# Kernel optimization log

Hardware: AMD Instinct MI355X
Metric: run time of the kernel (lower is better)

The kernel has to match this reference:

```python
import jax, jax.numpy as jnp
import numpy as np

NUM_HEADS = 12
NUM_GROUPS = 4
METRIC_SCALE = 1.0
CLS_MIX = 1.0
MEAN_MIX = 0.5
ROUTER_SCALE = 1.0
DIFF_SCALE = 1.0
B, N, D, HF = 16, 577, 768, 3072


def _ln(x, g, b, eps=1e-5):
    mu = jnp.mean(x, axis=-1, keepdims=True)
    var = jnp.mean(jnp.square(x - mu), axis=-1, keepdims=True)
    return (x - mu) * jax.lax.rsqrt(var + eps) * g + b


def setup_inputs() -> dict:
    key = jax.random.key(0)
    ks = iter(jax.random.split(key, 16))
    w = lambda shape, std: jax.random.normal(next(ks), shape, jnp.float32) * std
    return {
        "x": w((B, N, D), 1.0),
        "ln1_g": jnp.ones((D,)), "ln1_b": jnp.zeros((D,)),
        "ad_ln_g": jnp.ones((D,)), "ad_ln_b": jnp.zeros((D,)),
        "ad_w": w((D, D), 0.02),
        "w_qkv": w((D, 3 * D), 0.02),
        "w_proj": w((D, D), 0.02), "b_proj": jnp.zeros((D,)),
        "ln2_g": jnp.ones((D,)), "ln2_b": jnp.zeros((D,)),
        "fc1_w": w((D, HF), 0.02), "fc1_b": jnp.zeros((HF,)),
        "fc2_w": w((HF, D), 0.02), "fc2_b": jnp.zeros((D,)),
        "r_ln_g": jnp.ones((HF,)), "r_ln_b": jnp.zeros((HF,)),
        "r_proj_w": w((2 * HF, NUM_GROUPS), 0.02), "r_proj_b": jnp.zeros((NUM_GROUPS,)),
        "r_gate_w": w((2 * HF, 1), 0.02), "r_gate_b": jnp.full((1,), -2.0),
        "r_scale": jnp.full((NUM_GROUPS,), 0.1),
        "d_ln_g": jnp.ones((HF,)), "d_ln_b": jnp.zeros((HF,)),
        "d_out_w": w((HF, HF), 0.005),
        "d_gate_w": w((HF, 1), 0.02), "d_gate_b": jnp.full((1,), -1.5),
    }


def reference(x, ln1_g, ln1_b, ad_ln_g, ad_ln_b, ad_w, w_qkv, w_proj, b_proj,
              ln2_g, ln2_b, fc1_w, fc1_b, fc2_w, fc2_b,
              r_ln_g, r_ln_b, r_proj_w, r_proj_b, r_gate_w, r_gate_b, r_scale,
              d_ln_g, d_ln_b, d_out_w, d_gate_w, d_gate_b):
    b, n, d = x.shape
    hd = d // NUM_HEADS
    # ---- GeoAttention (pre-norm) ----
    h = _ln(x, ln1_g, ln1_b)
    # metric adapter: residual LN+Linear (SharedAttentionMetricAdapter)
    metric_h = h + METRIC_SCALE * (_ln(h, ad_ln_g, ad_ln_b) @ ad_w)
    # q,k from metric path; v from plain path (asymmetric Q/K vs V)
    qk = metric_h @ w_qkv[:, : 2 * d]                # [b,n,2d]
    v = h @ w_qkv[:, 2 * d :]                        # [b,n,d]
    q = qk[..., :d].reshape(b, n, NUM_HEADS, hd).transpose(0, 2, 1, 3)
    k = qk[..., d:].reshape(b, n, NUM_HEADS, hd).transpose(0, 2, 1, 3)
    v = v.reshape(b, n, NUM_HEADS, hd).transpose(0, 2, 1, 3)
    attn = jax.nn.softmax(jnp.einsum("bhnd,bhmd->bhnm", q, k) * (hd ** -0.5), axis=-1)
    out = jnp.einsum("bhnm,bhmd->bhnd", attn, v).transpose(0, 2, 1, 3).reshape(b, n, d)
    x = x + out @ w_proj + b_proj
    # ---- GeoMlp (pre-norm) ----
    h2 = _ln(x, ln2_g, ln2_b)
    hid = h2 @ fc1_w + fc1_b                         # [b,n,HF]
    # GroupCompetitionRouter on hidden
    rn = _ln(hid, r_ln_g, r_ln_b)
    summary = jnp.concatenate([CLS_MIX * rn[:, 0], MEAN_MIX * jnp.mean(rn[:, 1:], axis=1)], axis=-1)  # [b,2HF]
    wts = jax.nn.softmax(summary @ r_proj_w + r_proj_b, axis=-1)       # [b,G]
    gate = jax.nn.sigmoid(summary @ r_gate_w + r_gate_b)               # [b,1]
    centered = wts * float(NUM_GROUPS) - 1.0
    grouped = hid.reshape(b, n, NUM_GROUPS, HF // NUM_GROUPS)
    scale = 1.0 + ROUTER_SCALE * gate[:, None, :, None] * r_scale[None, None, :, None] * centered[:, None, :, None]
    hid = (grouped * scale).reshape(b, n, HF)
    # TokenDiffusionMixer on hidden
    dn = _ln(hid, d_ln_g, d_ln_b)
    tr = dn / jnp.maximum(jnp.linalg.norm(dn, axis=-1, keepdims=True), 1e-12)
    aff = jax.nn.softmax(jnp.einsum("bnc,bmc->bnm", tr, tr) * (HF ** -0.5), axis=-1)
    diffusion = jnp.einsum("bnm,bmc->bnc", aff, dn) - dn
    dgate = jax.nn.sigmoid(dn[:, 0] @ d_gate_w + d_gate_b)             # [b,1]
    hid = hid + DIFF_SCALE * dgate[:, :, None] * (diffusion @ d_out_w)
    # activation + fc2
    hid = jax.nn.gelu(hid, approximate=False)
    return x + hid @ fc2_w + fc2_b
```

## Files before the change

kernel.cpp:

```cpp
#include <hip/hip_runtime.h>
#include <math.h>

typedef unsigned short u16;
typedef unsigned int   u32;
typedef __attribute__((ext_vector_type(4))) float f32x4;
typedef __attribute__((ext_vector_type(4))) u32   u32x4;
typedef __attribute__((ext_vector_type(8))) short s16x8;

#define DEV __device__ __forceinline__
#define AS1 __attribute__((address_space(1)))
#define AS3 __attribute__((address_space(3)))

DEV float b2f(u16 u){ u32 x = ((u32)u)<<16; float f; __builtin_memcpy(&f,&x,4); return f; }
DEV u16 f2b(float f){ u32 x; __builtin_memcpy(&x,&f,4); u32 r = x + 0x7FFFu + ((x>>16)&1u); return (u16)(r>>16); }

DEV float ldf(const float* p, long i){ return p[i]; }
DEV float ldf(const u16*   p, long i){ return b2f(p[i]); }

DEV void gload16(const u16* g, u16* l){
  __builtin_amdgcn_global_load_lds((const AS1 u32*)(const void*)g,
                                   (AS3 u32*)(void*)l, 16, 0, 0);
}

DEV float wave_sum(float v){
#pragma unroll
  for(int o=32;o;o>>=1) v += __shfl_down(v,o,64);
  return v;
}
DEV float wave_max(float v){
#pragma unroll
  for(int o=32;o;o>>=1) v = fmaxf(v, __shfl_down(v,o,64));
  return v;
}
DEV float block_sum(float v, float* tmp){
  v = wave_sum(v);
  if((threadIdx.x&63)==0) tmp[threadIdx.x>>6]=v;
  __syncthreads();
  float r = tmp[0]+tmp[1]+tmp[2]+tmp[3];
  __syncthreads();
  return r;
}
DEV float block_max(float v, float* tmp){
  v = wave_max(v);
  if((threadIdx.x&63)==0) tmp[threadIdx.x>>6]=v;
  __syncthreads();
  float r = fmaxf(fmaxf(tmp[0],tmp[1]),fmaxf(tmp[2],tmp[3]));
  __syncthreads();
  return r;
}

template<typename TI>
__global__ void transpose_pad(const TI* __restrict__ in, u16* __restrict__ out,
                              int R, int C, int Rpad, long strideI, long strideO){
  __shared__ u16 t[32][33];
  in  += (long)blockIdx.z*strideI;
  out += (long)blockIdx.z*strideO;
  int tx = threadIdx.x & 31, ty = threadIdx.x >> 5;
  int bc = blockIdx.x*32, br = blockIdx.y*32;
#pragma unroll
  for(int i=0;i<32;i+=8){
    int r = br+ty+i, c = bc+tx;
    float v = (r<R && c<C) ? ldf(in,(long)r*C+c) : 0.f;
    t[ty+i][tx] = f2b(v);
  }
  __syncthreads();
#pragma unroll
  for(int i=0;i<32;i+=8){
    int c = bc+ty+i, r = br+tx;
    if(c<C && r<Rpad) out[(long)c*Rpad + r] = t[tx][ty+i];
  }
}

template<typename TI>
__global__ void ln_rows(const TI* __restrict__ x, const float* __restrict__ g,
                        const float* __restrict__ b, u16* __restrict__ y, int W){
  __shared__ float tmp[4];
  long base=(long)blockIdx.x*W;
  float s=0.f, ss=0.f;
  for(int c=threadIdx.x;c<W;c+=256){ float v=ldf(x,base+c); s+=v; ss+=v*v; }
  s=block_sum(s,tmp); ss=block_sum(ss,tmp);
  float mu=s/W;
  float rstd=rsqrtf(fmaxf(ss/W-mu*mu,0.f)+1e-5f);
  for(int c=threadIdx.x;c<W;c+=256){
    float v=ldf(x,base+c);
    y[base+c]=f2b((v-mu)*rstd*g[c]+b[c]);
  }
}

__global__ void ln2_rows(const float* __restrict__ x,
                         const float* __restrict__ g1, const float* __restrict__ b1,
                         const float* __restrict__ g2, const float* __restrict__ b2,
                         u16* __restrict__ h, u16* __restrict__ lnh){
  __shared__ float tmp[4];
  __shared__ float row[768];
  long base=(long)blockIdx.x*768;
  float s=0.f, ss=0.f;
  for(int c=threadIdx.x;c<768;c+=256){ float v=x[base+c]; s+=v; ss+=v*v; }
  s=block_sum(s,tmp); ss=block_sum(ss,tmp);
  float mu=s*(1.f/768.f);
  float rstd=rsqrtf(fmaxf(ss*(1.f/768.f)-mu*mu,0.f)+1e-5f);
  float s2=0.f, ss2=0.f;
  for(int c=threadIdx.x;c<768;c+=256){
    float v=(x[base+c]-mu)*rstd*g1[c]+b1[c];
    row[c]=v; h[base+c]=f2b(v);
    s2+=v; ss2+=v*v;
  }
  s2=block_sum(s2,tmp); ss2=block_sum(ss2,tmp);
  float mu2=s2*(1.f/768.f);
  float rstd2=rsqrtf(fmaxf(ss2*(1.f/768.f)-mu2*mu2,0.f)+1e-5f);
  for(int c=threadIdx.x;c<768;c+=256){
    lnh[base+c]=f2b((row[c]-mu2)*rstd2*g2[c]+b2[c]);
  }
}

__global__ void row_stats(const u16* __restrict__ x, float* __restrict__ stats, int W){
  __shared__ float tmp[4];
  long base=(long)blockIdx.x*W;
  float s=0.f,ss=0.f;
  for(int c=threadIdx.x;c<W;c+=256){ float v=b2f(x[base+c]); s+=v; ss+=v*v; }
  s=block_sum(s,tmp); ss=block_sum(ss,tmp);
  if(threadIdx.x==0){
    float mu=s/W;
    stats[2*(long)blockIdx.x]=mu;
    stats[2*(long)blockIdx.x+1]=rsqrtf(fmaxf(ss/W-mu*mu,0.f)+1e-5f);
  }
}

__global__ void dn_kernel(const u16* __restrict__ x, const float* __restrict__ g,
                          const float* __restrict__ b, const float* __restrict__ scalef,
                          u16* __restrict__ dn, float* __restrict__ rn){
  const int W=3072;
  __shared__ float tmp[4];
  __shared__ u16 rowb[3072];
  long row=(long)blockIdx.x;
  long base=row*(long)W;
  int bz=(int)(row/577);
  float s=0.f,ss=0.f;
  for(int c=threadIdx.x;c<W;c+=256){
    float sc=scalef[bz*4 + ((c>>8)/3)];
    float v=b2f(x[base+c])*sc;
    rowb[c]=f2b(v);
    s+=v; ss+=v*v;
  }
  s=block_sum(s,tmp); ss=block_sum(ss,tmp);
  float mu=s/W;
  float rstd=rsqrtf(fmaxf(ss/W-mu*mu,0.f)+1e-5f);
  float sq=0.f;
  for(int c=threadIdx.x;c<W;c+=256){
    float v=(b2f(rowb[c])-mu)*rstd*g[c]+b[c];
    sq+=v*v;
  }
  sq=block_sum(sq,tmp);
  float r=1.f/fmaxf(sqrtf(sq),1e-12f);
  for(int c=threadIdx.x;c<W;c+=256){
    float v=(b2f(rowb[c])-mu)*rstd*g[c]+b[c];
    dn[base+c]=f2b(v);
  }
  if(threadIdx.x==0) rn[blockIdx.x]=r;
}

__global__ void softmax_rows(u16* __restrict__ S, int W, int Wp,
                             const float* __restrict__ rs, int rpb, float alpha){
  __shared__ float tmp[4];
  long row = blockIdx.x;
  u16* p = S + row*(long)Wp;
  float rowscale = alpha;
  const float* rsb = nullptr;
  if(rs){ long bt=row/rpb; int m=(int)(row%rpb); rsb = rs + bt*(long)rpb; rowscale *= rsb[m]; }
  float mx=-3e38f;
  for(int c=threadIdx.x;c<W;c+=256){
    float v=b2f(p[c])*rowscale; if(rs) v*=rsb[c];
    mx=fmaxf(mx,v);
  }
  mx=block_max(mx,tmp);
  float sm=0.f;
  for(int c=threadIdx.x;c<W;c+=256){
    float v=b2f(p[c])*rowscale; if(rs) v*=rsb[c];
    sm+=__expf(v-mx);
  }
  sm=block_sum(sm,tmp);
  float inv=1.f/sm;
  for(int c=threadIdx.x;c<W;c+=256){
    float v=b2f(p[c])*rowscale; if(rs) v*=rsb[c];
    p[c]=f2b(__expf(v-mx)*inv);
  }
  for(int c=W+threadIdx.x;c<Wp;c+=256) p[c]=0;
}

__global__ void split_heads(const u16* __restrict__ qk, u16* __restrict__ qh, u16* __restrict__ kh){
  int i = blockIdx.x*256+threadIdx.x;
  if(i >= 16*577*12*8) return;
  int dv = i&7; int h=(i>>3)%12; int bn=i/96;
  int b=bn/577, n=bn%577;
  long src=(long)bn*1536 + h*64 + dv*8;
  long dst=((long)((b*12+h)*577+n))*64 + dv*8;
  *(u32x4*)(qh+dst) = *(const u32x4*)(qk+src);
  *(u32x4*)(kh+dst) = *(const u32x4*)(qk+src+768);
}
__global__ void merge_heads(const u16* __restrict__ aoh, u16* __restrict__ aout){
  int i = blockIdx.x*256+threadIdx.x;
  if(i >= 16*577*12*8) return;
  int dv=i&7; int h=(i>>3)%12; int bn=i/96;
  int b=bn/577, n=bn%577;
  long dst=(long)bn*768 + h*64 + dv*8;
  long src=((long)((b*12+h)*577+n))*64 + dv*8;
  *(u32x4*)(aout+dst) = *(const u32x4*)(aoh+src);
}
__global__ void make_vT(const u16* __restrict__ v, u16* __restrict__ vT){
  long i = (long)blockIdx.x*256+threadIdx.x;
  if(i >= (long)192*64*608) return;
  int n=(int)(i%608); long q=i/608; int d=(int)(q&63); int bh=(int)(q>>6);
  int b=bh/12, h=bh%12;
  u16 val=0;
  if(n<577) val = v[((long)(b*577+n))*768 + h*64 + d];
  vT[i]=val;
}

__global__ void summary_kernel(const u16* __restrict__ hid, const float* __restrict__ stats,
                               const float* __restrict__ rg, const float* __restrict__ rb,
                               float* __restrict__ summ){
  int b=blockIdx.y;
  int c=blockIdx.x*256+threadIdx.x;
  const u16* hb=hid+(size_t)b*577*3072;
  const float* st=stats+(size_t)b*577*2;
  float g=rg[c], be=rb[c];
  float cls=(b2f(hb[c])-st[0])*st[1]*g+be;
  float acc=0.f;
#pragma unroll 4
  for(int n=1;n<577;n++) acc += (b2f(hb[(size_t)n*3072+c])-st[2*n])*st[2*n+1];
  summ[(size_t)b*6144+c]        = 1.0f*cls;
  summ[(size_t)b*6144+3072+c]   = 0.5f*(g*(acc*(1.f/576.f))+be);
}

__global__ void router_kernel(const float* __restrict__ summ, const float* __restrict__ pw,
                              const float* __restrict__ pb, const float* __restrict__ gw,
                              const float* __restrict__ gb, const float* __restrict__ rsc,
                              float* __restrict__ scalef){
  __shared__ float tmp[4];
  int b=blockIdx.x;
  float a0=0,a1=0,a2=0,a3=0,a4=0;
  for(int c=threadIdx.x;c<6144;c+=256){
    float sv=summ[(size_t)b*6144+c];
    a0+=sv*pw[c*4+0]; a1+=sv*pw[c*4+1]; a2+=sv*pw[c*4+2]; a3+=sv*pw[c*4+3];
    a4+=sv*gw[c];
  }
  a0=block_sum(a0,tmp); a1=block_sum(a1,tmp); a2=block_sum(a2,tmp);
  a3=block_sum(a3,tmp); a4=block_sum(a4,tmp);
  if(threadIdx.x==0){
    float l0=a0+pb[0], l1=a1+pb[1], l2=a2+pb[2], l3=a3+pb[3];
    float mx=fmaxf(fmaxf(l0,l1),fmaxf(l2,l3));
    float e0=__expf(l0-mx),e1=__expf(l1-mx),e2=__expf(l2-mx),e3=__expf(l3-mx);
    float s=e0+e1+e2+e3;
    float gate=1.f/(1.f+__expf(-(a4+gb[0])));
    float w0=e0/s,w1=e1/s,w2=e2/s,w3=e3/s;
    scalef[b*4+0]=1.f+gate*rsc[0]*(4.f*w0-1.f);
    scalef[b*4+1]=1.f+gate*rsc[1]*(4.f*w1-1.f);
    scalef[b*4+2]=1.f+gate*rsc[2]*(4.f*w2-1.f);
    scalef[b*4+3]=1.f+gate*rsc[3]*(4.f*w3-1.f);
  }
}

__global__ void dgate_kernel(const u16* __restrict__ dn, const float* __restrict__ gw,
                             const float* __restrict__ gb, float* __restrict__ dgate){
  __shared__ float tmp[4];
  int b=blockIdx.x;
  const u16* row = dn + (size_t)b*577*3072;
  float a=0.f;
  for(int c=threadIdx.x;c<3072;c+=256) a+=b2f(row[c])*gw[c];
  a=block_sum(a,tmp);
  if(threadIdx.x==0) dgate[b]=1.f/(1.f+__expf(-(a+gb[0])));
}

constexpr int F_BIAS=1, F_RES=2, F_GELU=4, F_GATE=8, F_RESF32=16, F_OUTF32=32, F_SCRES=64;

DEV int swz(int u){ int row=u>>2, sl=u&3; return row*4 + (sl ^ ((row>>1)&3)); }

template<int FLAGS>
__global__ __launch_bounds__(256,2) void gemm_bt(
  const u16* __restrict__ A, long lda, long szA,
  const u16* __restrict__ B, long ldb, long szB,
  void* __restrict__ Cv, long ldc, long szC,
  const float* __restrict__ bias,
  const void* __restrict__ resv, long ldr, long szR, float res_scale,
  const float* __restrict__ gate,
  float alpha, int M, int N, int K, int NX, int NY)
{
  __shared__ alignas(16) u16 shA[128*32];
  __shared__ alignas(16) u16 shB[128*32];
  const int nwg = (int)gridDim.x;
  const int orig = (int)blockIdx.x;
  const int q = nwg>>3, r = nwg&7;
  const int xcd = orig&7, idx = orig>>3;
  const int wg = (xcd<r ? xcd*(q+1) : r*(q+1)+(xcd-r)*q) + idx;
  const int by = wg % NY; const int t_ = wg / NY;
  const int bx = t_ % NX; const int z  = t_ / NX;

  A += (long)z*szA; B += (long)z*szB;
  const int tid=threadIdx.x, lane=tid&63, wid=tid>>6;
  const int wr=wid>>1, wc=wid&1;
  const long m0=(long)bx*128, n0=(long)by*128;
  f32x4 acc[4][4];
#pragma unroll
  for(int i=0;i<4;i++)
#pragma unroll
    for(int j=0;j<4;j++){ f32x4 zv={0.f,0.f,0.f,0.f}; acc[i][j]=zv; }

  const int lr = lane>>2, lsl = lane&3;
  const u16* pA[2]; const u16* pB[2]; u16* lA[2]; u16* lB[2];
#pragma unroll
  for(int i=0;i<2;i++){
    int ra = wid*32 + i*16 + lr;
    int kc = (lsl ^ ((ra>>1)&3))*8;
    long gr = m0+ra; if(gr>=M) gr=M-1;
    long gb = n0+ra; if(gb>=N) gb=N-1;
    pA[i] = A + gr*lda + kc;
    pB[i] = B + gb*ldb + kc;
    lA[i] = shA + (wid*32 + i*16)*32;
    lB[i] = shB + (wid*32 + i*16)*32;
  }

  for(int k0=0;k0<K;k0+=32){
    __syncthreads();
#pragma unroll
    for(int i=0;i<2;i++){
      gload16(pA[i]+k0, lA[i]);
      gload16(pB[i]+k0, lB[i]);
    }
    __syncthreads();
    const int ks = lane>>4, rr = lane&15;
    s16x8 av[4], bv[4];
#pragma unroll
    for(int mi=0;mi<4;mi++) av[mi] = ((const s16x8*)shA)[swz((wr*64+mi*16+rr)*4+ks)];
#pragma unroll
    for(int ni=0;ni<4;ni++) bv[ni] = ((const s16x8*)shB)[swz((wc*64+ni*16+rr)*4+ks)];
#pragma unroll
    for(int mi=0;mi<4;mi++)
#pragma unroll
      for(int ni=0;ni<4;ni++)
        acc[mi][ni] = __builtin_amdgcn_mfma_f32_16x16x32_bf16(av[mi], bv[ni], acc[mi][ni], 0,0,0);
  }
  const float* resf = (const float*)resv + (long)z*szR;
  const u16*   resh = (const u16*)resv   + (long)z*szR;
  float* Cf = (float*)Cv + (long)z*szC;
  u16*   Ch = (u16*)Cv   + (long)z*szC;
  float gv = (FLAGS&F_GATE)? gate[z] : 1.f;
#pragma unroll
  for(int mi=0;mi<4;mi++){
#pragma unroll
    for(int ni=0;ni<4;ni++){
      long c0 = n0 + wc*64 + ni*16 + (lane&15);
      if(c0>=N) continue;
      float bb = (FLAGS&F_BIAS)? bias[c0] : 0.f;
#pragma unroll
      for(int r2=0;r2<4;r2++){
        long rw = m0 + wr*64 + mi*16 + (lane>>4)*4 + r2;
        if(rw>=M) continue;
        float t = acc[mi][ni][r2]*alpha*gv + bb;
        if(FLAGS&F_RES){
          float rvv = (FLAGS&F_RESF32)? resf[rw*ldr+c0] : b2f(resh[rw*ldr+c0]);
          t += res_scale*rvv;
        }
        if(FLAGS&F_GELU) t = 0.5f*t*(1.f+erff(t*0.70710678118654752f));
        if(FLAGS&F_OUTF32) Cf[rw*ldc+c0]=t;
        else               Ch[rw*ldc+c0]=f2b(t);
      }
    }
  }
}

static inline int gpack(int M,int N,int nb,int& NX,int& NY){
  NX=(M+127)/128; NY=(N+127)/128; return NX*NY*nb;
}

template<int FLAGS>
__global__ __launch_bounds__(512,2) void gemm256(
  const u16* __restrict__ A, long lda,
  const u16* __restrict__ B, long ldb,
  void* __restrict__ Cv, long ldc,
  const float* __restrict__ bias,
  const void* __restrict__ resv, long ldr,
  const float* __restrict__ gate, const float* __restrict__ scres,
  float irpz, float alpha, int M, int N, int K, int NY)
{
  __shared__ alignas(16) u16 smem[65536];
  char* sm=(char*)smem;
  const int nwg=(int)gridDim.x, orig=(int)blockIdx.x;
  const int qq=nwg>>3, rr8=nwg&7, xcd=orig&7, idx=orig>>3;
  const int wg=(xcd<rr8? xcd*(qq+1): rr8*(qq+1)+(xcd-rr8)*qq)+idx;
  const int by=wg%NY, bx=wg/NY;
  const long m0=(long)bx*256, n0=(long)by*256;
  const int tid=threadIdx.x, lane=tid&63, wid=tid>>6;
  const int wr=wid>>2, wc=wid&3, l15=lane&15, ks=lane>>4;

  f32x4 acc[8][4];
#pragma unroll
  for(int i=0;i<8;i++)
#pragma unroll
    for(int j=0;j<4;j++){ f32x4 zv={0.f,0.f,0.f,0.f}; acc[i][j]=zv; }

  const u16 *sA[2][2], *sB[2][2];
  int dstj[2];
#pragma unroll
  for(int j=0;j<2;j++){
    int u=j*512+tid, row=u>>3;
    long co=(long)(((u&7)^(row&7))*8);
    dstj[j]=u*16;
#pragma unroll
    for(int h=0;h<2;h++){
      long gr=m0+h*128+row; if(gr>=M) gr=M-1;
      long gb=n0+h*128+row; if(gb>=N) gb=N-1;
      sA[h][j]=A+gr*lda+co;
      sB[h][j]=B+gb*ldb+co;
    }
  }
  int xsl[2]; xsl[0]=((ks^(l15&7))<<4); xsl[1]=(((4+ks)^(l15&7))<<4);
  const int arow = wr*16384 + l15*128;
  int brow[4];
#pragma unroll
  for(int nj=0;nj<4;nj++){ int n=wc*64+nj*16; brow[nj]=32768+(n>>7)*16384+((n&127)+l15)*128; }
  const int NT=K>>6;

#define STG(P,mat,h,kt,bf) { \
  gload16(P[h][0]+(long)(kt)*64,(u16*)(sm+(bf)*65536+(mat)*32768+(h)*16384+dstj[0])); \
  gload16(P[h][1]+(long)(kt)*64,(u16*)(sm+(bf)*65536+(mat)*32768+(h)*16384+dstj[1])); }
#define BAR() { asm volatile("":::"memory"); __builtin_amdgcn_s_barrier(); asm volatile("":::"memory"); }
#define LGKM() { asm volatile("s_waitcnt lgkmcnt(0)":::"memory"); __builtin_amdgcn_sched_barrier(0); }
#define MFMA16(A0,KB) { \
  __builtin_amdgcn_s_setprio(1); \
  _Pragma("unroll") for(int i_=0;i_<4;i_++) \
  _Pragma("unroll") for(int j_=0;j_<4;j_++) \
    acc[(A0)+i_][j_] = __builtin_amdgcn_mfma_f32_16x16x32_bf16(av[i_], bv[KB][j_], acc[(A0)+i_][j_], 0,0,0); \
  __builtin_amdgcn_s_setprio(0); }

  STG(sA,0,0,0,0); STG(sA,0,1,0,0); STG(sB,1,0,0,0); STG(sB,1,1,0,0);
  STG(sB,1,0,1,1); STG(sB,1,1,1,1);
  asm volatile("s_waitcnt vmcnt(4)":::"memory");
  BAR();

  s16x8 av[4], bv[2][4];
  for(int t=0;t<NT;++t){
    const int cur=t&1, nxt=cur^1;
    const char* bp = sm + cur*65536;
#pragma unroll
    for(int kk=0;kk<2;kk++)
#pragma unroll
      for(int nj=0;nj<4;nj++) bv[kk][nj]=*(const s16x8*)(bp+brow[nj]+xsl[kk]);
#pragma unroll
    for(int i=0;i<4;i++) av[i]=*(const s16x8*)(bp+arow+i*2048+xsl[0]);
    if(t+1<NT){ STG(sA,0,0,t+1,nxt); STG(sA,0,1,t+1,nxt); }
    BAR();
    LGKM();
    MFMA16(0,0);
    BAR();
#pragma unroll
    for(int i=0;i<4;i++) av[i]=*(const s16x8*)(bp+arow+(4+i)*2048+xsl[0]);
    BAR();
    LGKM();
    MFMA16(4,0);
    BAR();
#pragma unroll
    for(int i=0;i<4;i++) av[i]=*(const s16x8*)(bp+arow+i*2048+xsl[1]);
    if(t+2<NT) STG(sB,1,0,t+2,cur);
    BAR();
    LGKM();
    MFMA16(0,1);
    BAR();
#pragma unroll
    for(int i=0;i<4;i++) av[i]=*(const s16x8*)(bp+arow+(4+i)*2048+xsl[1]);
    if(t+2<NT) STG(sB,1,1,t+2,cur);
    if(t+2<NT) asm volatile("s_waitcnt vmcnt(4)":::"memory");
    else       asm volatile("s_waitcnt vmcnt(0)":::"memory");
    BAR();
    LGKM();
    MFMA16(4,1);
    BAR();
  }
#undef STG
#undef BAR
#undef LGKM
#undef MFMA16

  const float* resf=(const float*)resv; const u16* resh=(const u16*)resv;
  float* Cf=(float*)Cv; u16* Ch=(u16*)Cv;
#pragma unroll
  for(int mf=0;mf<8;mf++){
#pragma unroll
    for(int j=0;j<4;j++){
      long c0 = n0 + wc*64 + j*16 + l15;
      float bb=(FLAGS&F_BIAS)? bias[c0]:0.f;
      int cg=((int)(c0>>8))/3;
#pragma unroll
      for(int r2=0;r2<4;r2++){
        long rw = m0 + wr*128 + mf*16 + ks*4 + r2;
        if(rw>=M) continue;
        float t=acc[mf][j][r2]*alpha;
        if(FLAGS&(F_GATE|F_SCRES)){
          int z=(int)(((float)rw+0.5f)*irpz);
          if(FLAGS&F_GATE) t*=gate[z];
          if(FLAGS&F_SCRES) t += scres[z*4+cg]*b2f(resh[rw*ldr+c0]);
        } else if(FLAGS&F_RES){
          float rvv=(FLAGS&F_RESF32)? resf[rw*ldr+c0] : b2f(resh[rw*ldr+c0]);
          t += rvv;
        }
        t+=bb;
        if(FLAGS&F_GELU) t=0.5f*t*(1.f+erff(t*0.70710678118654752f));
        if(FLAGS&F_OUTF32) Cf[rw*ldc+c0]=t;
        else               Ch[rw*ldc+c0]=f2b(t);
      }
    }
  }
}

extern "C" void kernel_launch(void* const* d_in, const int* in_sizes, int n_in,
                              void* d_out, int out_size, void* d_ws, size_t ws_size,
                              hipStream_t stream){
  const int BNr=16*577;
  const float* x      = (const float*)d_in[0];
  const float* ln1_g  = (const float*)d_in[1];
  const float* ln1_b  = (const float*)d_in[2];
  const float* ad_ln_g= (const float*)d_in[3];
  const float* ad_ln_b= (const float*)d_in[4];
  const float* ad_w   = (const float*)d_in[5];
  const float* w_qkv  = (const float*)d_in[6];
  const float* w_proj = (const float*)d_in[7];
  const float* b_proj = (const float*)d_in[8];
  const float* ln2_g  = (const float*)d_in[9];
  const float* ln2_b  = (const float*)d_in[10];
  const float* fc1_w  = (const float*)d_in[11];
  const float* fc1_b  = (const float*)d_in[12];
  const float* fc2_w  = (const float*)d_in[13];
  const float* fc2_b  = (const float*)d_in[14];
  const float* r_ln_g = (const float*)d_in[15];
  const float* r_ln_b = (const float*)d_in[16];
  const float* r_proj_w=(const float*)d_in[17];
  const float* r_proj_b=(const float*)d_in[18];
  const float* r_gate_w=(const float*)d_in[19];
  const float* r_gate_b=(const float*)d_in[20];
  const float* r_scale =(const float*)d_in[21];
  const float* d_ln_g = (const float*)d_in[22];
  const float* d_ln_b = (const float*)d_in[23];
  const float* d_outw = (const float*)d_in[24];
  const float* d_gate_w=(const float*)d_in[25];
  const float* d_gate_b=(const float*)d_in[26];

  char* ws=(char*)d_ws;
  size_t off=0;
  auto take=[&](size_t nb){ size_t r=off; off=(off+nb+255)&~(size_t)255; return r; };
  auto al  =[&](size_t v){ return (v+255)&~(size_t)255; };
  const size_t o_qkvT = take((size_t)2304*768*2);
  const size_t o_adT  = take((size_t)768*768*2);
  const size_t o_projT= take((size_t)768*768*2);
  const size_t o_fc1T = take((size_t)3072*768*2);
  const size_t o_fc2T = take((size_t)768*3072*2);
  const size_t o_doutT= take((size_t)3072*3072*2);
  const size_t o_x2   = take((size_t)BNr*768*4);
  const size_t o_hid  = take((size_t)BNr*3072*2);
  const size_t o_stats= take((size_t)BNr*2*4);
  const size_t o_rn   = take((size_t)BNr*4);
  const size_t o_sum  = take((size_t)16*6144*4);
  const size_t o_scalef=take(64*4);
  const size_t o_dg   = take(64);
  const size_t o_h    = take((size_t)BNr*768*2);
  const size_t o_lnh  = take((size_t)BNr*768*2);
  const size_t o_metric=take((size_t)BNr*768*2);
  const size_t o_qk   = take((size_t)BNr*1536*2);
  const size_t o_v    = take((size_t)BNr*768*2);
  const size_t o_qh   = take((size_t)192*577*64*2);
  const size_t o_kh   = take((size_t)192*577*64*2);
  const size_t o_vT   = take((size_t)192*64*608*2);
  (void)o_v; (void)o_vT; (void)in_sizes; (void)n_in; (void)out_size;
  const size_t o_S    = o_qk;
  const size_t o_aoh  = o_metric;
  const size_t o_aout = o_h;
  const size_t o_h2   = o_lnh;
  const size_t o_dn   = o_h;
  const size_t o_aff  = al(o_dn + (size_t)BNr*3072*2);
  const size_t o_dnTb = al(o_aff + (size_t)16*577*608*2);
  const size_t o_diff = al(o_dnTb + (size_t)4*3072*608*2);
  const size_t o_hact = o_dn;
  size_t endA = off;
  size_t endB = o_diff + (size_t)BNr*3072*2;
  const size_t o_big = al(endA > endB ? endA : endB);
  const size_t big_need = (size_t)192*577*608*2;
  const bool bigws = ws_size >= o_big + big_need;

  u16* qkvT=(u16*)(ws+o_qkvT); u16* adT=(u16*)(ws+o_adT); u16* projT=(u16*)(ws+o_projT);
  u16* fc1T=(u16*)(ws+o_fc1T); u16* fc2T=(u16*)(ws+o_fc2T); u16* doutT=(u16*)(ws+o_doutT);
  float* x2=(float*)(ws+o_x2); u16* hid=(u16*)(ws+o_hid);
  float* stats=(float*)(ws+o_stats); float* rn=(float*)(ws+o_rn);
  float* summ=(float*)(ws+o_sum); float* scalef=(float*)(ws+o_scalef); float* dgate=(float*)(ws+o_dg);
  u16* hbuf=(u16*)(ws+o_h); u16* lnh=(u16*)(ws+o_lnh); u16* metric=(u16*)(ws+o_metric);
  u16* qkbuf=(u16*)(ws+o_qk); u16* vbuf=(u16*)(ws+o_v);
  u16* qh=(u16*)(ws+o_qh); u16* kh=(u16*)(ws+o_kh); u16* vT=(u16*)(ws+o_vT);
  u16* Sc=(u16*)(ws+o_S); u16* aoh=(u16*)(ws+o_aoh); u16* aout=(u16*)(ws+o_aout);
  u16* h2=(u16*)(ws+o_h2);
  u16* dn=(u16*)(ws+o_dn); u16* aff=(u16*)(ws+o_aff); u16* dnTb=(u16*)(ws+o_dnTb);
  u16* diff=(u16*)(ws+o_diff); u16* hact=(u16*)(ws+o_hact);
  u16* Sf=(u16*)(ws+o_big); u16* dnTbF=(u16*)(ws+o_big);

  dim3 blk(256), blk5(512);
  int NX, NY, ng;
  transpose_pad<float><<<dim3(72,24,1),blk,0,stream>>>(w_qkv, qkvT, 768,2304,768, 0,0);
  transpose_pad<float><<<dim3(24,24,1),blk,0,stream>>>(ad_w,  adT,  768,768, 768, 0,0);
  transpose_pad<float><<<dim3(24,24,1),blk,0,stream>>>(w_proj,projT,768,768, 768, 0,0);
  transpose_pad<float><<<dim3(96,24,1),blk,0,stream>>>(fc1_w, fc1T, 768,3072,768, 0,0);
  transpose_pad<float><<<dim3(24,96,1),blk,0,stream>>>(fc2_w, fc2T, 3072,768,3072,0,0);
  transpose_pad<float><<<dim3(96,96,1),blk,0,stream>>>(d_outw,doutT,3072,3072,3072,0,0);
  ln2_rows<<<BNr,blk,0,stream>>>(x, ln1_g, ln1_b, ad_ln_g, ad_ln_b, hbuf, lnh);
  ng=gpack(BNr,768,1,NX,NY);
  gemm_bt<F_RES><<<ng,blk,0,stream>>>(lnh,768,0, adT,768,0, metric,768,0,
      nullptr, hbuf,768,0, 1.f, nullptr, 1.f, BNr,768,768, NX,NY);
  gemm256<0><<<dim3(37*6),blk5,0,stream>>>(metric,768, qkvT,768, qkbuf,1536,
      nullptr, nullptr,0, nullptr,nullptr, 0.f, 1.f, BNr,1536,768, 6);
  ng=gpack(BNr,768,1,NX,NY);
  gemm_bt<0><<<ng,blk,0,stream>>>(hbuf,768,0, qkvT+(size_t)1536*768,768,0, vbuf,768,0,
      nullptr, nullptr,0,0,0.f, nullptr, 1.f, BNr,768,768, NX,NY);
  split_heads<<<3462,blk,0,stream>>>(qkbuf, qh, kh);
  make_vT<<<29184,blk,0,stream>>>(vbuf, vT);
  if(bigws){
    ng=gpack(577,577,192,NX,NY);
    gemm_bt<0><<<ng,blk,0,stream>>>(qh,64,(long)577*64, kh,64,(long)577*64,
        Sf,608,(long)577*608, nullptr, nullptr,0,0,0.f, nullptr, 0.125f, 577,577,64, NX,NY);
    softmax_rows<<<192*577,blk,0,stream>>>(Sf,577,608, nullptr,577, 1.f);
    ng=gpack(577,64,192,NX,NY);
    gemm_bt<0><<<ng,blk,0,stream>>>(Sf,608,(long)577*608, vT,608,(long)64*608,
        aoh,64,(long)577*64, nullptr, nullptr,0,0,0.f, nullptr, 1.f, 577,64,608, NX,NY);
  } else {
    for(int c=0;c<6;c++){
      const u16* qc=qh+(size_t)c*32*577*64;
      const u16* kc=kh+(size_t)c*32*577*64;
      ng=gpack(577,577,32,NX,NY);
      gemm_bt<0><<<ng,blk,0,stream>>>(qc,64,(long)577*64, kc,64,(long)577*64,
          Sc,608,(long)577*608, nullptr, nullptr,0,0,0.f, nullptr, 0.125f, 577,577,64, NX,NY);
      softmax_rows<<<32*577,blk,0,stream>>>(Sc,577,608, nullptr,577, 1.f);
      ng=gpack(577,64,32,NX,NY);
      gemm_bt<0><<<ng,blk,0,stream>>>(Sc,608,(long)577*608, vT+(size_t)c*32*64*608,608,(long)64*608,
          aoh+(size_t)c*32*577*64,64,(long)577*64, nullptr, nullptr,0,0,0.f, nullptr, 1.f, 577,64,608, NX,NY);
    }
  }
  merge_heads<<<3462,blk,0,stream>>>(aoh, aout);
  ng=gpack(BNr,768,1,NX,NY);
  gemm_bt<F_RES|F_BIAS|F_RESF32|F_OUTF32><<<ng,blk,0,stream>>>(aout,768,0, projT,768,0,
      x2,768,0, b_proj, x,768,0, 1.f, nullptr, 1.f, BNr,768,768, NX,NY);
  ln_rows<float><<<BNr,blk,0,stream>>>(x2, ln2_g, ln2_b, h2, 768);
  gemm256<F_BIAS><<<dim3(37*12),blk5,0,stream>>>(h2,768, fc1T,768, hid,3072,
      fc1_b, nullptr,0, nullptr,nullptr, 0.f, 1.f, BNr,3072,768, 12);
  row_stats<<<BNr,blk,0,stream>>>(hid, stats, 3072);
  summary_kernel<<<dim3(12,16),blk,0,stream>>>(hid, stats, r_ln_g, r_ln_b, summ);
  router_kernel<<<16,blk,0,stream>>>(summ, r_proj_w, r_proj_b, r_gate_w, r_gate_b, r_scale, scalef);
  dn_kernel<<<BNr,blk,0,stream>>>(hid, d_ln_g, d_ln_b, scalef, dn, rn);
  dgate_kernel<<<16,blk,0,stream>>>(dn, d_gate_w, d_gate_b, dgate);
  ng=gpack(577,577,16,NX,NY);
  gemm_bt<0><<<ng,blk,0,stream>>>(dn,3072,(long)577*3072, dn,3072,(long)577*3072,
      aff,608,(long)577*608, nullptr, nullptr,0,0,0.f, nullptr, 1.f, 577,577,3072, NX,NY);
  softmax_rows<<<BNr,blk,0,stream>>>(aff,577,608, rn,577, 0.01804219634f);
  if(bigws){
    transpose_pad<u16><<<dim3(96,19,16),blk,0,stream>>>(dn, dnTbF,
        577,3072,608, (long)577*3072, (long)3072*608);
    ng=gpack(577,3072,16,NX,NY);
    gemm_bt<F_RES><<<ng,blk,0,stream>>>(aff,608,(long)577*608,
        dnTbF,608,(long)3072*608, diff,3072,(long)577*3072,
        nullptr, dn,3072,(long)577*3072, -1.f, nullptr, 1.f, 577,3072,608, NX,NY);
  } else {
    for(int g4=0; g4<4; ++g4){
      transpose_pad<u16><<<dim3(96,19,4),blk,0,stream>>>(dn+(size_t)g4*4*577*3072, dnTb,
          577,3072,608, (long)577*3072, (long)3072*608);
      ng=gpack(577,3072,4,NX,NY);
      gemm_bt<F_RES><<<ng,blk,0,stream>>>(aff+(size_t)g4*4*577*608,608,(long)577*608,
          dnTb,608,(long)3072*608, diff+(size_t)g4*4*577*3072,3072,(long)577*3072,
          nullptr, dn+(size_t)g4*4*577*3072,3072,(long)577*3072, -1.f, nullptr, 1.f, 577,3072,608, NX,NY);
    }
  }
  gemm256<F_GELU|F_GATE|F_SCRES><<<dim3(37*12),blk5,0,stream>>>(diff,3072, doutT,3072,
      hact,3072, nullptr, hid,3072, dgate, scalef, 1.f/577.f, 1.f, BNr,3072,3072, 12);
  ng=gpack(BNr,768,1,NX,NY);
  gemm_bt<F_RES|F_BIAS|F_RESF32|F_OUTF32><<<ng,blk,0,stream>>>(hact,3072,0,
      fc2T,3072,0, d_out,768,0, fc2_b, x2,768,0, 1.f, nullptr, 1.f, BNr,768,3072, NX,NY);
}
```

Baseline: 1.530 ms.

## Replace double-buffered 256x256 GEMM mainloop with single-buffer K=32 loop

Swaps the hand-pipelined, double-buffered 256x256 GEMM mainloop (64-wide K tiles, staggered async LDS loads, setprio) for a simple single-buffered loop over 32-wide K tiles with two __syncthreads per iteration. LDS use drops from 128KB to 32KB and launch bounds are raised to allow 4 blocks per CU, relying on occupancy instead of software pipelining to hide latency. The 8x4 accumulator array per thread stays, so register pressure may keep 4 blocks from fitting. Global loads are also no longer overlapped with MFMA within a block, and a column bound check is added in the epilogue.

```diff
diff --git a/kernel.cpp b/kernel.cpp
--- a/kernel.cpp
+++ b/kernel.cpp
@@ -373,7 +373,7 @@
 }
 
 template<int FLAGS>
-__global__ __launch_bounds__(512,2) void gemm256(
+__global__ __launch_bounds__(512,4) void gemm256(
   const u16* __restrict__ A, long lda,
   const u16* __restrict__ B, long ldb,
   void* __restrict__ Cv, long ldc,
@@ -382,8 +382,8 @@
   const float* __restrict__ gate, const float* __restrict__ scres,
   float irpz, float alpha, int M, int N, int K, int NY)
 {
-  __shared__ alignas(16) u16 smem[65536];
-  char* sm=(char*)smem;
+  __shared__ alignas(16) u16 shA[256*32];
+  __shared__ alignas(16) u16 shB[256*32];
   const int nwg=(int)gridDim.x, orig=(int)blockIdx.x;
   const int qq=nwg>>3, rr8=nwg&7, xcd=orig&7, idx=orig>>3;
   const int wg=(xcd<rr8? xcd*(qq+1): rr8*(qq+1)+(xcd-rr8)*qq)+idx;
@@ -398,87 +398,38 @@
 #pragma unroll
     for(int j=0;j<4;j++){ f32x4 zv={0.f,0.f,0.f,0.f}; acc[i][j]=zv; }
 
-  const u16 *sA[2][2], *sB[2][2];
-  int dstj[2];
+  const u16* pA[2]; const u16* pB[2]; u16* lA[2]; u16* lB[2];
 #pragma unroll
   for(int j=0;j<2;j++){
-    int u=j*512+tid, row=u>>3;
-    long co=(long)(((u&7)^(row&7))*8);
-    dstj[j]=u*16;
-#pragma unroll
-    for(int h=0;h<2;h++){
-      long gr=m0+h*128+row; if(gr>=M) gr=M-1;
-      long gb=n0+h*128+row; if(gb>=N) gb=N-1;
-      sA[h][j]=A+gr*lda+co;
-      sB[h][j]=B+gb*ldb+co;
+    int u=j*512+tid, row=u>>2;
+    int kc=((u&3)^((row>>1)&3))*8;
+    long gr=m0+row; if(gr>=M) gr=M-1;
+    long gb=n0+row; if(gb>=N) gb=N-1;
+    pA[j]=A+gr*lda+kc;
+    pB[j]=B+gb*ldb+kc;
+    lA[j]=shA+u*8;
+    lB[j]=shB+u*8;
+  }
+
+  for(int k0=0;k0<K;k0+=32){
+    __syncthreads();
+#pragma unroll
+    for(int j=0;j<2;j++){
+      gload16(pA[j]+k0, lA[j]);
+      gload16(pB[j]+k0, lB[j]);
     }
-  }
-  int xsl[2]; xsl[0]=((ks^(l15&7))<<4); xsl[1]=(((4+ks)^(l15&7))<<4);
-  const int arow = wr*16384 + l15*128;
-  int brow[4];
-#pragma unroll
-  for(int nj=0;nj<4;nj++){ int n=wc*64+nj*16; brow[nj]=32768+(n>>7)*16384+((n&127)+l15)*128; }
-  const int NT=K>>6;
-
-#define STG(P,mat,h,kt,bf) { \
-  gload16(P[h][0]+(long)(kt)*64,(u16*)(sm+(bf)*65536+(mat)*32768+(h)*16384+dstj[0])); \
-  gload16(P[h][1]+(long)(kt)*64,(u16*)(sm+(bf)*65536+(mat)*32768+(h)*16384+dstj[1])); }
-#define BAR() { asm volatile("":::"memory"); __builtin_amdgcn_s_barrier(); asm volatile("":::"memory"); }
-#define LGKM() { asm volatile("s_waitcnt lgkmcnt(0)":::"memory"); __builtin_amdgcn_sched_barrier(0); }
-#define MFMA16(A0,KB) { \
-  __builtin_amdgcn_s_setprio(1); \
-  _Pragma("unroll") for(int i_=0;i_<4;i_++) \
-  _Pragma("unroll") for(int j_=0;j_<4;j_++) \
-    acc[(A0)+i_][j_] = __builtin_amdgcn_mfma_f32_16x16x32_bf16(av[i_], bv[KB][j_], acc[(A0)+i_][j_], 0,0,0); \
-  __builtin_amdgcn_s_setprio(0); }
-
-  STG(sA,0,0,0,0); STG(sA,0,1,0,0); STG(sB,1,0,0,0); STG(sB,1,1,0,0);
-  STG(sB,1,0,1,1); STG(sB,1,1,1,1);
-  asm volatile("s_waitcnt vmcnt(4)":::"memory");
-  BAR();
-
-  s16x8 av[4], bv[2][4];
-  for(int t=0;t<NT;++t){
-    const int cur=t&1, nxt=cur^1;
-    const char* bp = sm + cur*65536;
-#pragma unroll
-    for(int kk=0;kk<2;kk++)
-#pragma unroll
-      for(int nj=0;nj<4;nj++) bv[kk][nj]=*(const s16x8*)(bp+brow[nj]+xsl[kk]);
-#pragma unroll
-    for(int i=0;i<4;i++) av[i]=*(const s16x8*)(bp+arow+i*2048+xsl[0]);
-    if(t+1<NT){ STG(sA,0,0,t+1,nxt); STG(sA,0,1,t+1,nxt); }
-    BAR();
-    LGKM();
-    MFMA16(0,0);
-    BAR();
-#pragma unroll
-    for(int i=0;i<4;i++) av[i]=*(const s16x8*)(bp+arow+(4+i)*2048+xsl[0]);
-    BAR();
-    LGKM();
-    MFMA16(4,0);
-    BAR();
-#pragma unroll
-    for(int i=0;i<4;i++) av[i]=*(const s16x8*)(bp+arow+i*2048+xsl[1]);
-    if(t+2<NT) STG(sB,1,0,t+2,cur);
-    BAR();
-    LGKM();
-    MFMA16(0,1);
-    BAR();
-#pragma unroll
-    for(int i=0;i<4;i++) av[i]=*(const s16x8*)(bp+arow+(4+i)*2048+xsl[1]);
-    if(t+2<NT) STG(sB,1,1,t+2,cur);
-    if(t+2<NT) asm volatile("s_waitcnt vmcnt(4)":::"memory");
-    else       asm volatile("s_waitcnt vmcnt(0)":::"memory");
-    BAR();
-    LGKM();
-    MFMA16(4,1);
-    BAR();
-  }
-#undef STG
-#undef BAR
-#undef LGKM
-#undef MFMA16
+    __syncthreads();
+    s16x8 av[8], bv[4];
+#pragma unroll
+    for(int nj=0;nj<4;nj++) bv[nj] = ((const s16x8*)shB)[swz((wc*64+nj*16+l15)*4+ks)];
+#pragma unroll
+    for(int mi=0;mi<8;mi++) av[mi] = ((const s16x8*)shA)[swz((wr*128+mi*16+l15)*4+ks)];
+#pragma unroll
+    for(int mi=0;mi<8;mi++)
+#pragma unroll
+      for(int nj=0;nj<4;nj++)
+        acc[mi][nj] = __builtin_amdgcn_mfma_f32_16x16x32_bf16(av[mi], bv[nj], acc[mi][nj], 0,0,0);
+  }
 
   const float* resf=(const float*)resv; const u16* resh=(const u16*)resv;
   float* Cf=(float*)Cv; u16* Ch=(u16*)Cv;
@@ -487,6 +438,7 @@
 #pragma unroll
     for(int j=0;j<4;j++){
       long c0 = n0 + wc*64 + j*16 + l15;
+      if(c0>=N) continue;
       float bb=(FLAGS&F_BIAS)? bias[c0]:0.f;
       int cg=((int)(c0>>8))/3;
 #pragma unroll
```

Result: slower. 2.967 ms (+93.9%).

## Fuse head-split into QK GEMM epilogue and drop big-workspace attention path

Applied to the files above, without the earlier changes.

The QK projection GEMM now writes Q and K directly in per-head layout through a new epilogue flag, removing the separate split_heads kernel and its extra read/write pass. The big-workspace single-launch attention and diffusion paths are removed, so the chunked loops always run. This saves memory traffic, but the epilogue stores become scattered, and if the batched path was previously active it trades one large launch for several smaller ones.

```diff
diff --git a/kernel.cpp b/kernel.cpp
--- a/kernel.cpp
+++ b/kernel.cpp
@@ -187,16 +187,6 @@
   for(int c=W+threadIdx.x;c<Wp;c+=256) p[c]=0;
 }
 
-__global__ void split_heads(const u16* __restrict__ qk, u16* __restrict__ qh, u16* __restrict__ kh){
-  int i = blockIdx.x*256+threadIdx.x;
-  if(i >= 16*577*12*8) return;
-  int dv = i&7; int h=(i>>3)%12; int bn=i/96;
-  int b=bn/577, n=bn%577;
-  long src=(long)bn*1536 + h*64 + dv*8;
-  long dst=((long)((b*12+h)*577+n))*64 + dv*8;
-  *(u32x4*)(qh+dst) = *(const u32x4*)(qk+src);
-  *(u32x4*)(kh+dst) = *(const u32x4*)(qk+src+768);
-}
 __global__ void merge_heads(const u16* __restrict__ aoh, u16* __restrict__ aout){
   int i = blockIdx.x*256+threadIdx.x;
   if(i >= 16*577*12*8) return;
@@ -271,7 +261,7 @@
   if(threadIdx.x==0) dgate[b]=1.f/(1.f+__expf(-(a+gb[0])));
 }
 
-constexpr int F_BIAS=1, F_RES=2, F_GELU=4, F_GATE=8, F_RESF32=16, F_OUTF32=32, F_SCRES=64;
+constexpr int F_BIAS=1, F_RES=2, F_GELU=4, F_GATE=8, F_RESF32=16, F_OUTF32=32, F_SCRES=64, F_QKH=128;
 
 DEV int swz(int u){ int row=u>>2, sl=u&3; return row*4 + (sl ^ ((row>>1)&3)); }
 
@@ -494,6 +484,16 @@
         long rw = m0 + wr*128 + mf*16 + ks*4 + r2;
         if(rw>=M) continue;
         float t=acc[mf][j][r2]*alpha;
+        if(FLAGS&F_QKH){
+          int z=(int)(((float)rw+0.5f)*irpz);
+          int n=(int)(rw - (long)z*577);
+          int hh=(int)(c0>>6);
+          int d=(int)(c0&63);
+          int h12 = (hh<12)? hh : hh-12;
+          long dst=((long)((z*12+h12)*577+n))*64 + d + (hh<12 ? 0L : (long)192*577*64);
+          Ch[dst]=f2b(t);
+          continue;
+        }
         if(FLAGS&(F_GATE|F_SCRES)){
           int z=(int)(((float)rw+0.5f)*irpz);
           if(FLAGS&F_GATE) t*=gate[z];
@@ -568,7 +568,7 @@
   const size_t o_qh   = take((size_t)192*577*64*2);
   const size_t o_kh   = take((size_t)192*577*64*2);
   const size_t o_vT   = take((size_t)192*64*608*2);
-  (void)o_v; (void)o_vT; (void)in_sizes; (void)n_in; (void)out_size;
+  (void)o_v; (void)o_vT; (void)o_kh; (void)ws_size; (void)in_sizes; (void)n_in; (void)out_size;
   const size_t o_S    = o_qk;
   const size_t o_aoh  = o_metric;
   const size_t o_aout = o_h;
@@ -578,11 +578,6 @@
   const size_t o_dnTb = al(o_aff + (size_t)16*577*608*2);
   const size_t o_diff = al(o_dnTb + (size_t)4*3072*608*2);
   const size_t o_hact = o_dn;
-  size_t endA = off;
-  size_t endB = o_diff + (size_t)BNr*3072*2;
-  const size_t o_big = al(endA > endB ? endA : endB);
-  const size_t big_need = (size_t)192*577*608*2;
-  const bool bigws = ws_size >= o_big + big_need;
 
   u16* qkvT=(u16*)(ws+o_qkvT); u16* adT=(u16*)(ws+o_adT); u16* projT=(u16*)(ws+o_projT);
   u16* fc1T=(u16*)(ws+o_fc1T); u16* fc2T=(u16*)(ws+o_fc2T); u16* doutT=(u16*)(ws+o_doutT);
@@ -590,13 +585,12 @@
   float* stats=(float*)(ws+o_stats); float* rn=(float*)(ws+o_rn);
   float* summ=(float*)(ws+o_sum); float* scalef=(float*)(ws+o_scalef); float* dgate=(float*)(ws+o_dg);
   u16* hbuf=(u16*)(ws+o_h); u16* lnh=(u16*)(ws+o_lnh); u16* metric=(u16*)(ws+o_metric);
-  u16* qkbuf=(u16*)(ws+o_qk); u16* vbuf=(u16*)(ws+o_v);
+  u16* vbuf=(u16*)(ws+o_v);
   u16* qh=(u16*)(ws+o_qh); u16* kh=(u16*)(ws+o_kh); u16* vT=(u16*)(ws+o_vT);
   u16* Sc=(u16*)(ws+o_S); u16* aoh=(u16*)(ws+o_aoh); u16* aout=(u16*)(ws+o_aout);
   u16* h2=(u16*)(ws+o_h2);
   u16* dn=(u16*)(ws+o_dn); u16* aff=(u16*)(ws+o_aff); u16* dnTb=(u16*)(ws+o_dnTb);
   u16* diff=(u16*)(ws+o_diff); u16* hact=(u16*)(ws+o_hact);
-  u16* Sf=(u16*)(ws+o_big); u16* dnTbF=(u16*)(ws+o_big);
 
   dim3 blk(256), blk5(512);
   int NX, NY, ng;
@@ -610,33 +604,22 @@
   ng=gpack(BNr,768,1,NX,NY);
   gemm_bt<F_RES><<<ng,blk,0,stream>>>(lnh,768,0, adT,768,0, metric,768,0,
       nullptr, hbuf,768,0, 1.f, nullptr, 1.f, BNr,768,768, NX,NY);
-  gemm256<0><<<dim3(37*6),blk5,0,stream>>>(metric,768, qkvT,768, qkbuf,1536,
-      nullptr, nullptr,0, nullptr,nullptr, 0.f, 1.f, BNr,1536,768, 6);
+  gemm256<F_QKH><<<dim3(37*6),blk5,0,stream>>>(metric,768, qkvT,768, qh,0,
+      nullptr, nullptr,0, nullptr,nullptr, 1.f/577.f, 1.f, BNr,1536,768, 6);
   ng=gpack(BNr,768,1,NX,NY);
   gemm_bt<0><<<ng,blk,0,stream>>>(hbuf,768,0, qkvT+(size_t)1536*768,768,0, vbuf,768,0,
       nullptr, nullptr,0,0,0.f, nullptr, 1.f, BNr,768,768, NX,NY);
-  split_heads<<<3462,blk,0,stream>>>(qkbuf, qh, kh);
   make_vT<<<29184,blk,0,stream>>>(vbuf, vT);
-  if(bigws){
-    ng=gpack(577,577,192,NX,NY);
-    gemm_bt<0><<<ng,blk,0,stream>>>(qh,64,(long)577*64, kh,64,(long)577*64,
-        Sf,608,(long)577*608, nullptr, nullptr,0,0,0.f, nullptr, 0.125f, 577,577,64, NX,NY);
-    softmax_rows<<<192*577,blk,0,stream>>>(Sf,577,608, nullptr,577, 1.f);
-    ng=gpack(577,64,192,NX,NY);
-    gemm_bt<0><<<ng,blk,0,stream>>>(Sf,608,(long)577*608, vT,608,(long)64*608,
-        aoh,64,(long)577*64, nullptr, nullptr,0,0,0.f, nullptr, 1.f, 577,64,608, NX,NY);
-  } else {
-    for(int c=0;c<6;c++){
-      const u16* qc=qh+(size_t)c*32*577*64;
-      const u16* kc=kh+(size_t)c*32*577*64;
-      ng=gpack(577,577,32,NX,NY);
-      gemm_bt<0><<<ng,blk,0,stream>>>(qc,64,(long)577*64, kc,64,(long)577*64,
-          Sc,608,(long)577*608, nullptr, nullptr,0,0,0.f, nullptr, 0.125f, 577,577,64, NX,NY);
-      softmax_rows<<<32*577,blk,0,stream>>>(Sc,577,608, nullptr,577, 1.f);
-      ng=gpack(577,64,32,NX,NY);
-      gemm_bt<0><<<ng,blk,0,stream>>>(Sc,608,(long)577*608, vT+(size_t)c*32*64*608,608,(long)64*608,
-          aoh+(size_t)c*32*577*64,64,(long)577*64, nullptr, nullptr,0,0,0.f, nullptr, 1.f, 577,64,608, NX,NY);
-    }
+  for(int c=0;c<6;c++){
+    const u16* qc=qh+(size_t)c*32*577*64;
+    const u16* kc=kh+(size_t)c*32*577*64;
+    ng=gpack(577,577,32,NX,NY);
+    gemm_bt<0><<<ng,blk,0,stream>>>(qc,64,(long)577*64, kc,64,(long)577*64,
+        Sc,608,(long)577*608, nullptr, nullptr,0,0,0.f, nullptr, 0.125f, 577,577,64, NX,NY);
+    softmax_rows<<<32*577,blk,0,stream>>>(Sc,577,608, nullptr,577, 1.f);
+    ng=gpack(577,64,32,NX,NY);
+    gemm_bt<0><<<ng,blk,0,stream>>>(Sc,608,(long)577*608, vT+(size_t)c*32*64*608,608,(long)64*608,
+        aoh+(size_t)c*32*577*64,64,(long)577*64, nullptr, nullptr,0,0,0.f, nullptr, 1.f, 577,64,608, NX,NY);
   }
   merge_heads<<<3462,blk,0,stream>>>(aoh, aout);
   ng=gpack(BNr,768,1,NX,NY);
@@ -654,22 +637,13 @@
   gemm_bt<0><<<ng,blk,0,stream>>>(dn,3072,(long)577*3072, dn,3072,(long)577*3072,
       aff,608,(long)577*608, nullptr, nullptr,0,0,0.f, nullptr, 1.f, 577,577,3072, NX,NY);
   softmax_rows<<<BNr,blk,0,stream>>>(aff,577,608, rn,577, 0.01804219634f);
-  if(bigws){
-    transpose_pad<u16><<<dim3(96,19,16),blk,0,stream>>>(dn, dnTbF,
+  for(int g4=0; g4<4; ++g4){
+    transpose_pad<u16><<<dim3(96,19,4),blk,0,stream>>>(dn+(size_t)g4*4*577*3072, dnTb,
         577,3072,608, (long)577*3072, (long)3072*608);
-    ng=gpack(577,3072,16,NX,NY);
-    gemm_bt<F_RES><<<ng,blk,0,stream>>>(aff,608,(long)577*608,
-        dnTbF,608,(long)3072*608, diff,3072,(long)577*3072,
-        nullptr, dn,3072,(long)577*3072, -1.f, nullptr, 1.f, 577,3072,608, NX,NY);
-  } else {
-    for(int g4=0; g4<4; ++g4){
-      transpose_pad<u16><<<dim3(96,19,4),blk,0,stream>>>(dn+(size_t)g4*4*577*3072, dnTb,
-          577,3072,608, (long)577*3072, (long)3072*608);
-      ng=gpack(577,3072,4,NX,NY);
-      gemm_bt<F_RES><<<ng,blk,0,stream>>>(aff+(size_t)g4*4*577*608,608,(long)577*608,
-          dnTb,608,(long)3072*608, diff+(size_t)g4*4*577*3072,3072,(long)577*3072,
-          nullptr, dn+(size_t)g4*4*577*3072,3072,(long)577*3072, -1.f, nullptr, 1.f, 577,3072,608, NX,NY);
-    }
+    ng=gpack(577,3072,4,NX,NY);
+    gemm_bt<F_RES><<<ng,blk,0,stream>>>(aff+(size_t)g4*4*577*608,608,(long)577*608,
+        dnTb,608,(long)3072*608, diff+(size_t)g4*4*577*3072,3072,(long)577*3072,
+        nullptr, dn+(size_t)g4*4*577*3072,3072,(long)577*3072, -1.f, nullptr, 1.f, 577,3072,608, NX,NY);
   }
   gemm256<F_GELU|F_GATE|F_SCRES><<<dim3(37*12),blk5,0,stream>>>(diff,3072, doutT,3072,
       hact,3072, nullptr, hid,3072, dgate, scalef, 1.f/577.f, 1.f, BNr,3072,3072, 12);
```

Result: no change. 1.525 ms (-0.3%).
